# Performance work log

Measured on AMD Instinct MI355X. Metric: run time of the kernel, lower is better.

The kernel has to match this reference:

```python
import jax, jax.numpy as jnp
import numpy as np

C, H, OUT = 64, 128, 64          # in_channels, hidden_dim, out_channels
N, E = 20000, 640000             # nodes, edges
LN_EPS = 1e-5


def layer_norm(x, g, b):
    mu = jnp.mean(x, axis=-1, keepdims=True)
    var = jnp.var(x, axis=-1, keepdims=True)
    return (x - mu) * jax.lax.rsqrt(var + LN_EPS) * g + b


def setup_inputs() -> dict:
    key = jax.random.key(0)
    ks = jax.random.split(key, 12)
    F = 2 * C + 5  # edge MLP input dim = 133

    def w(k, shape, fan_in):
        return jax.random.normal(k, shape, jnp.float32) / np.float32(np.sqrt(fan_in))

    return {
        "x": jax.random.normal(ks[0], (N, C), jnp.float32),
        "pos": jax.random.normal(ks[1], (N, 2), jnp.float32),
        "vel": jax.random.normal(ks[2], (N, 2), jnp.float32),
        # phi_e: Linear(F,H) -> LN -> Softplus -> Linear(H,H) -> Softplus -> Linear(H,H)
        "We1": w(ks[3], (F, H), F), "be1": jnp.zeros((H,), jnp.float32),
        "ge1": jnp.ones((H,), jnp.float32), "bte1": jnp.zeros((H,), jnp.float32),
        "We2": w(ks[4], (H, H), H), "be2": jnp.zeros((H,), jnp.float32),
        "We3": w(ks[5], (H, H), H), "be3": jnp.zeros((H,), jnp.float32),
        # phi_v: Linear(F,H) -> LN -> Softplus -> Linear(H,1)
        "Wv1": w(ks[6], (F, H), F), "bv1": jnp.zeros((H,), jnp.float32),
        "gv1": jnp.ones((H,), jnp.float32), "btv1": jnp.zeros((H,), jnp.float32),
        "Wv2": w(ks[7], (H, 1), H), "bv2": jnp.zeros((1,), jnp.float32),
        # phi_h: Linear(C+H+1,H) -> LN -> Softplus -> Linear(H,OUT)
        "Wh1": w(ks[8], (C + H + 1, H), C + H + 1), "bh1": jnp.zeros((H,), jnp.float32),
        "gh1": jnp.ones((H,), jnp.float32), "bth1": jnp.zeros((H,), jnp.float32),
        "Wh2": w(ks[9], (H, OUT), H), "bh2": jnp.zeros((OUT,), jnp.float32),
        "edge_index": jax.random.randint(ks[10], (2, E), 0, N, dtype=jnp.int64)
        if jax.config.jax_enable_x64 else jax.random.randint(ks[10], (2, E), 0, N, dtype=jnp.int32),
    }


def reference(x, pos, vel,
              We1, be1, ge1, bte1, We2, be2, We3, be3,
              Wv1, bv1, gv1, btv1, Wv2, bv2,
              Wh1, bh1, gh1, bth1, Wh2, bh2,
              edge_index):
    src = edge_index[0]  # j (source / x_j)
    dst = edge_index[1]  # i (target / x_i, aggregation index)

    # per-edge geometric features (gather)
    rel_pos = pos[src] - pos[dst]                                   # [E,2]
    rel_vel = vel[src] - vel[dst]                                   # [E,2]
    dist_sq = jnp.sum(rel_pos ** 2, axis=-1, keepdims=True)         # [E,1]
    dot_vr = jnp.sum(rel_vel * rel_pos, axis=-1, keepdims=True)     # [E,1]
    r2_inv = jnp.minimum(1.0 / (dist_sq + 0.05), 20.0)
    r6_inv = jnp.minimum(r2_inv ** 3, 400.0)
    r12_inv = jnp.minimum(r6_inv ** 2, 160000.0)

    tmp = jnp.concatenate([x[dst], x[src], dist_sq, dot_vr,
                           r2_inv, r6_inv, r12_inv], axis=1)        # [E, 2C+5]

    # phi_e (edge MLP)
    h = jax.nn.softplus(layer_norm(tmp @ We1 + be1, ge1, bte1))
    h = jax.nn.softplus(h @ We2 + be2)
    m_h_e = h @ We3 + be3                                           # [E,H]

    # phi_v (scalar weight on rel_pos -> equivariant vector message)
    v = jax.nn.softplus(layer_norm(tmp @ Wv1 + bv1, gv1, btv1))
    v_w = v @ Wv2 + bv2                                             # [E,1]
    m_v_e = v_w * rel_pos                                           # [E,2]

    # scatter-mean aggregation to target nodes
    n_nodes = x.shape[0]
    ones = jnp.ones((src.shape[0], 1), x.dtype)
    cnt = jax.ops.segment_sum(ones, dst, num_segments=n_nodes)
    denom = jnp.maximum(cnt, 1.0)
    m_h = jax.ops.segment_sum(m_h_e, dst, num_segments=n_nodes) / denom   # [N,H]
    m_v = jax.ops.segment_sum(m_v_e, dst, num_segments=n_nodes) / denom   # [N,2]

    m_v_norm = jnp.sqrt(jnp.sum((m_v + 1e-8) ** 2, axis=-1, keepdims=True))  # [N,1]

    # phi_h (node update MLP); shortcut is Identity since C == OUT
    hin = jnp.concatenate([x, m_h, m_v_norm], axis=-1)              # [N, C+H+1]
    hu = jax.nn.softplus(layer_norm(hin @ Wh1 + bh1, gh1, bth1))
    h_update = hu @ Wh2 + bh2                                       # [N,OUT]
    return x + h_update
```

## Files before the change

kernel.cpp:

```cpp
#include <hip/hip_runtime.h>
#include <stdint.h>

#define NCH    64
#define HID    128
#define OUTC   64
#define NNODE  20000
#define NEDGE  640000
#define FDIM   133
#define PHIN   193
#define TE     32
#define TN     32
#define NST    36
#define LN_EPS 1e-5f
#define KP1    160
#define KP2    128
#define CAG    132

typedef __attribute__((ext_vector_type(8))) short bf16x8;
typedef __attribute__((ext_vector_type(4))) float f32x4;

__device__ __forceinline__ unsigned short f2bf(float f) {
    union { float f; unsigned int i; } v; v.f = f;
    unsigned int b = v.i;
    return (unsigned short)((b + 0x7FFFu + ((b >> 16) & 1u)) >> 16);
}
__device__ __forceinline__ float sp(float xv) {
    return fmaxf(xv, 0.f) + __logf(1.0f + __expf(-fabsf(xv)));
}
__device__ __forceinline__ void atomAddF(float* p, float v) {
    __hip_atomic_fetch_add(p, v, __ATOMIC_RELAXED, __HIP_MEMORY_SCOPE_AGENT);
}
__device__ __forceinline__ int fragOff(int ks, int mt, int lanepos) {
    return ((ks * 2 + mt) * 64 + lanepos) * 8;
}

#define WT_WE1 0
#define WT_WV1 (128 * KP1)
#define WT_WE2 (2 * 128 * KP1)
#define WT_WE3 (2 * 128 * KP1 + 128 * KP2)
#define WT_TOTAL (2 * 128 * KP1 + 2 * 128 * KP2)

__global__ __launch_bounds__(256)
void eg_prep(const float* __restrict__ We1, const float* __restrict__ Wv1,
             const float* __restrict__ We2, const float* __restrict__ We3,
             short* __restrict__ wt)
{
    int idx = blockIdx.x * 256 + threadIdx.x;
    if (idx >= WT_TOTAL) return;
    if (idx < WT_WV1) {
        int n = idx / KP1, k = idx % KP1;
        wt[idx] = (k < FDIM) ? (short)f2bf(We1[(size_t)k * HID + n]) : (short)0;
    } else if (idx < WT_WE2) {
        int r = idx - WT_WV1; int n = r / KP1, k = r % KP1;
        wt[idx] = (k < FDIM) ? (short)f2bf(Wv1[(size_t)k * HID + n]) : (short)0;
    } else if (idx < WT_WE3) {
        int r = idx - WT_WE2; int n = r / KP2, k = r % KP2;
        wt[idx] = (short)f2bf(We2[(size_t)k * HID + n]);
    } else {
        int r = idx - WT_WE3; int n = r / KP2, k = r % KP2;
        wt[idx] = (short)f2bf(We3[(size_t)k * HID + n]);
    }
}

__global__ __launch_bounds__(256)
void eg_hist(const int* __restrict__ ei, int* __restrict__ deg)
{
    int i = blockIdx.x * 256 + threadIdx.x;
    if (i < NEDGE)
        __hip_atomic_fetch_add(&deg[ei[NEDGE + i]], 1, __ATOMIC_RELAXED, __HIP_MEMORY_SCOPE_AGENT);
}

__global__ __launch_bounds__(1024)
void eg_scan(const int* __restrict__ deg, int* __restrict__ cur)
{
    __shared__ int part[1024];
    const int tid = threadIdx.x;
    const int chunk = (NNODE + 1023) / 1024;
    const int base = tid * chunk;
    const int lim = min(base + chunk, NNODE);
    int s = 0;
    for (int j = base; j < lim; ++j) s += deg[j];
    part[tid] = s;
    __syncthreads();
    for (int off = 1; off < 1024; off <<= 1) {
        int v = (tid >= off) ? part[tid - off] : 0;
        __syncthreads();
        part[tid] += v;
        __syncthreads();
    }
    int run = (tid > 0) ? part[tid - 1] : 0;
    for (int j = base; j < lim; ++j) { cur[j] = run; run += deg[j]; }
}

__global__ __launch_bounds__(256)
void eg_scatter(const int* __restrict__ ei, int* __restrict__ cur,
                int* __restrict__ perm)
{
    int i = blockIdx.x * 256 + threadIdx.x;
    if (i < NEDGE) {
        int d = ei[NEDGE + i];
        int p = __hip_atomic_fetch_add(&cur[d], 1, __ATOMIC_RELAXED, __HIP_MEMORY_SCOPE_AGENT);
        perm[p] = i;
    }
}

__global__ __launch_bounds__(256, 5)
void eg_edge(const float* __restrict__ x, const float* __restrict__ pos,
             const float* __restrict__ vel,
             const float* __restrict__ be1, const float* __restrict__ ge1,
             const float* __restrict__ bte1, const float* __restrict__ be2,
             const float* __restrict__ be3,
             const float* __restrict__ bv1, const float* __restrict__ gv1,
             const float* __restrict__ btv1,
             const float* __restrict__ Wv2, const float* __restrict__ bv2,
             const short* __restrict__ wt,
             const int* __restrict__ ei, const int* __restrict__ perm,
             float* __restrict__ mh, float* __restrict__ mv)
{
    __shared__ __align__(16) short frag_s[5 * 2 * 64 * 8];
    __shared__ __align__(16) float cagg_s[TE * CAG];
    __shared__ float psum_s[512];
    __shared__ float mu_s[64], rs_s[64];
    __shared__ int   dst_s[TE], src_s[TE];
    __shared__ float rel_s[TE * 2], vw_s[TE];

    const int tid  = threadIdx.x;
    const int lane = tid & 63;
    const int wid  = tid >> 6;
    const int lr   = lane & 15;
    const int quad = lane >> 4;
    const int n0w  = wid * 32;
    const int e_base = blockIdx.x * TE;

    const short* We1T = wt + WT_WE1;
    const short* Wv1T = wt + WT_WV1;
    const short* We2T = wt + WT_WE2;
    const short* We3T = wt + WT_WE3;

    float geo[5];
    if (tid < TE) {
        int gi = perm[e_base + tid];
        int eS = ei[gi];
        int eD = ei[NEDGE + gi];
        src_s[tid] = eS; dst_s[tid] = eD;
        float rx = pos[2 * eS]     - pos[2 * eD];
        float ry = pos[2 * eS + 1] - pos[2 * eD + 1];
        float vx = vel[2 * eS]     - vel[2 * eD];
        float vy = vel[2 * eS + 1] - vel[2 * eD + 1];
        float dsq = rx * rx + ry * ry;
        float dvr = vx * rx + vy * ry;
        float r2  = fminf(1.0f / (dsq + 0.05f), 20.0f);
        float r6  = fminf(r2 * r2 * r2, 400.0f);
        float r12 = fminf(r6 * r6, 160000.0f);
        geo[0] = dsq; geo[1] = dvr; geo[2] = r2; geo[3] = r6; geo[4] = r12;
        rel_s[2 * tid] = rx; rel_s[2 * tid + 1] = ry;
    }
    if (tid < 128) {
        int4 z = {0, 0, 0, 0};
        *(int4*)&frag_s[4 * 2 * 64 * 8 + tid * 8] = z;
    }
    __syncthreads();

    if (tid < TE) {
        int off = fragOff(4, tid >> 4, (tid & 15));
        #pragma unroll
        for (int j = 0; j < 5; ++j) frag_s[off + j] = (short)f2bf(geo[j]);
    }
    {
        const int e = tid & 31, slot = tid >> 5;
        const int d = dst_s[e], s = src_s[e];
        #pragma unroll
        for (int h = 0; h < 2; ++h) {
            int o = slot + h * 8;
            int node = h ? s : d;
            int c0 = (o & 7) * 8;
            const float4 a0 = *(const float4*)&x[(size_t)node * NCH + c0];
            const float4 a1 = *(const float4*)&x[(size_t)node * NCH + c0 + 4];
            bf16x8 v;
            v[0] = (short)f2bf(a0.x); v[1] = (short)f2bf(a0.y);
            v[2] = (short)f2bf(a0.z); v[3] = (short)f2bf(a0.w);
            v[4] = (short)f2bf(a1.x); v[5] = (short)f2bf(a1.y);
            v[6] = (short)f2bf(a1.z); v[7] = (short)f2bf(a1.w);
            int ks = o >> 2, kq = o & 3;
            *(bf16x8*)&frag_s[fragOff(ks, e >> 4, kq * 16 + (e & 15))] = v;
        }
    }
    __syncthreads();

    const int ncol0 = n0w + lr;
    const int ncol1 = n0w + 16 + lr;

    f32x4 zero4 = {0.f, 0.f, 0.f, 0.f};
    f32x4 accE[2][2], accV[2][2];
    #pragma unroll
    for (int mt = 0; mt < 2; ++mt)
        #pragma unroll
        for (int nt = 0; nt < 2; ++nt) { accE[mt][nt] = zero4; accV[mt][nt] = zero4; }
    for (int ks = 0; ks < 5; ++ks) {
        bf16x8 af0 = *(const bf16x8*)&frag_s[fragOff(ks, 0, lane)];
        bf16x8 af1 = *(const bf16x8*)&frag_s[fragOff(ks, 1, lane)];
        int krow = ks * 32 + quad * 8;
        #pragma unroll
        for (int nt = 0; nt < 2; ++nt) {
            int n = n0w + nt * 16 + lr;
            bf16x8 bwE = *(const bf16x8*)&We1T[n * KP1 + krow];
            bf16x8 bwV = *(const bf16x8*)&Wv1T[n * KP1 + krow];
            accE[0][nt] = __builtin_amdgcn_mfma_f32_16x16x32_bf16(af0, bwE, accE[0][nt], 0, 0, 0);
            accE[1][nt] = __builtin_amdgcn_mfma_f32_16x16x32_bf16(af1, bwE, accE[1][nt], 0, 0, 0);
            accV[0][nt] = __builtin_amdgcn_mfma_f32_16x16x32_bf16(af0, bwV, accV[0][nt], 0, 0, 0);
            accV[1][nt] = __builtin_amdgcn_mfma_f32_16x16x32_bf16(af1, bwV, accV[1][nt], 0, 0, 0);
        }
    }
    {
        float be0 = be1[ncol0], be_1 = be1[ncol1];
        float bv0 = bv1[ncol0], bv_1 = bv1[ncol1];
        #pragma unroll
        for (int mt = 0; mt < 2; ++mt)
            #pragma unroll
            for (int r = 0; r < 4; ++r) {
                accE[mt][0][r] += be0; accE[mt][1][r] += be_1;
                accV[mt][0][r] += bv0; accV[mt][1][r] += bv_1;
            }
    }

    #pragma unroll
    for (int mt = 0; mt < 2; ++mt)
        #pragma unroll
        for (int r = 0; r < 4; ++r) {
            float se = accE[mt][0][r] + accE[mt][1][r];
            float qe = accE[mt][0][r] * accE[mt][0][r] + accE[mt][1][r] * accE[mt][1][r];
            float sv = accV[mt][0][r] + accV[mt][1][r];
            float qv = accV[mt][0][r] * accV[mt][0][r] + accV[mt][1][r] * accV[mt][1][r];
            #pragma unroll
            for (int m = 1; m < 16; m <<= 1) {
                se += __shfl_xor(se, m, 16);
                qe += __shfl_xor(qe, m, 16);
                sv += __shfl_xor(sv, m, 16);
                qv += __shfl_xor(qv, m, 16);
            }
            if (lr == 0) {
                int row = mt * 16 + quad * 4 + r;
                psum_s[      row * 4 + wid] = se;
                psum_s[128 + row * 4 + wid] = qe;
                psum_s[256 + row * 4 + wid] = sv;
                psum_s[384 + row * 4 + wid] = qv;
            }
        }
    __syncthreads();
    if (tid < 64) {
        int p = tid >> 5, row = tid & 31;
        float s = 0.f, q = 0.f;
        #pragma unroll
        for (int w = 0; w < 4; ++w) {
            s += psum_s[p * 256 +       row * 4 + w];
            q += psum_s[p * 256 + 128 + row * 4 + w];
        }
        float mu = s * (1.0f / HID);
        float var = q * (1.0f / HID) - mu * mu;
        mu_s[p * 32 + row] = mu;
        rs_s[p * 32 + row] = rsqrtf(var + LN_EPS);
    }
    __syncthreads();

    {
        float gE0 = ge1[ncol0], gE1 = ge1[ncol1];
        float tE0 = bte1[ncol0], tE1 = bte1[ncol1];
        float gV0 = gv1[ncol0], gV1 = gv1[ncol1];
        float tV0 = btv1[ncol0], tV1 = btv1[ncol1];
        float w20 = Wv2[ncol0], w21 = Wv2[ncol1];
        int ks0 = ncol0 >> 5, kq0 = (ncol0 & 31) >> 3, j0 = ncol0 & 7;
        int ks1 = ncol1 >> 5, kq1 = (ncol1 & 31) >> 3, j1 = ncol1 & 7;
        int fo0 = (ks0 * 128 + kq0 * 16) * 8 + j0;
        int fo1 = (ks1 * 128 + kq1 * 16) * 8 + j1;
        #pragma unroll
        for (int mt = 0; mt < 2; ++mt)
            #pragma unroll
            for (int r = 0; r < 4; ++r) {
                int rlow = quad * 4 + r, row = mt * 16 + rlow;
                float mu = mu_s[row], rsv = rs_s[row];
                float muV = mu_s[32 + row], rsV = rs_s[32 + row];
                float h0 = sp((accE[mt][0][r] - mu) * rsv * gE0 + tE0);
                float h1 = sp((accE[mt][1][r] - mu) * rsv * gE1 + tE1);
                frag_s[fo0 + (mt * 64 + rlow) * 8] = (short)f2bf(h0);
                frag_s[fo1 + (mt * 64 + rlow) * 8] = (short)f2bf(h1);
                float v0 = sp((accV[mt][0][r] - muV) * rsV * gV0 + tV0);
                float v1 = sp((accV[mt][1][r] - muV) * rsV * gV1 + tV1);
                float vp = v0 * w20 + v1 * w21;
                #pragma unroll
                for (int m = 1; m < 16; m <<= 1) vp += __shfl_xor(vp, m, 16);
                if (lr == 0) psum_s[row * 4 + wid] = vp;
            }
    }
    __syncthreads();
    if (tid < TE) {
        float s = 0.f;
        #pragma unroll
        for (int w = 0; w < 4; ++w) s += psum_s[tid * 4 + w];
        vw_s[tid] = s + bv2[0];
    }

    {
        f32x4 acc2[2][2];
        #pragma unroll
        for (int mt = 0; mt < 2; ++mt)
            #pragma unroll
            for (int nt = 0; nt < 2; ++nt) acc2[mt][nt] = zero4;
        for (int ks = 0; ks < 4; ++ks) {
            bf16x8 af0 = *(const bf16x8*)&frag_s[fragOff(ks, 0, lane)];
            bf16x8 af1 = *(const bf16x8*)&frag_s[fragOff(ks, 1, lane)];
            int krow = ks * 32 + quad * 8;
            #pragma unroll
            for (int nt = 0; nt < 2; ++nt) {
                int n = n0w + nt * 16 + lr;
                bf16x8 bw = *(const bf16x8*)&We2T[n * KP2 + krow];
                acc2[0][nt] = __builtin_amdgcn_mfma_f32_16x16x32_bf16(af0, bw, acc2[0][nt], 0, 0, 0);
                acc2[1][nt] = __builtin_amdgcn_mfma_f32_16x16x32_bf16(af1, bw, acc2[1][nt], 0, 0, 0);
            }
        }
        __syncthreads();
        #pragma unroll
        for (int nt = 0; nt < 2; ++nt) {
            int kg = n0w + nt * 16 + lr;
            float b2 = be2[kg];
            int ks = kg >> 5, kq = (kg & 31) >> 3, j = kg & 7;
            #pragma unroll
            for (int mt = 0; mt < 2; ++mt)
                #pragma unroll
                for (int r = 0; r < 4; ++r) {
                    short v = (short)f2bf(sp(acc2[mt][nt][r] + b2));
                    frag_s[fragOff(ks, mt, kq * 16 + quad * 4 + r) + j] = v;
                }
        }
    }
    __syncthreads();

    {
        f32x4 acc3[2][2];
        #pragma unroll
        for (int mt = 0; mt < 2; ++mt)
            #pragma unroll
            for (int nt = 0; nt < 2; ++nt) acc3[mt][nt] = zero4;
        for (int ks = 0; ks < 4; ++ks) {
            bf16x8 af0 = *(const bf16x8*)&frag_s[fragOff(ks, 0, lane)];
            bf16x8 af1 = *(const bf16x8*)&frag_s[fragOff(ks, 1, lane)];
            int krow = ks * 32 + quad * 8;
            #pragma unroll
            for (int nt = 0; nt < 2; ++nt) {
                int n = n0w + nt * 16 + lr;
                bf16x8 bw = *(const bf16x8*)&We3T[n * KP2 + krow];
                acc3[0][nt] = __builtin_amdgcn_mfma_f32_16x16x32_bf16(af0, bw, acc3[0][nt], 0, 0, 0);
                acc3[1][nt] = __builtin_amdgcn_mfma_f32_16x16x32_bf16(af1, bw, acc3[1][nt], 0, 0, 0);
            }
        }
        #pragma unroll
        for (int nt = 0; nt < 2; ++nt) {
            int n = n0w + nt * 16 + lr;
            float b3 = be3[n];
            #pragma unroll
            for (int mt = 0; mt < 2; ++mt)
                #pragma unroll
                for (int r = 0; r < 4; ++r) {
                    int m = mt * 16 + quad * 4 + r;
                    cagg_s[m * CAG + n] = acc3[mt][nt][r] + b3;
                }
        }
    }
    __syncthreads();

    {
        const int c = tid & 127, h = tid >> 7;
        const int m0 = h * 16;
        float run = cagg_s[m0 * CAG + c];
        int curd = dst_s[m0];
        #pragma unroll
        for (int m = m0 + 1; m < m0 + 16; ++m) {
            int d = dst_s[m];
            float v = cagg_s[m * CAG + c];
            if (d == curd) run += v;
            else { atomAddF(&mh[(size_t)curd * HID + c], run); curd = d; run = v; }
        }
        atomAddF(&mh[(size_t)curd * HID + c], run);
    }
    if (tid < 2) {
        const int c = tid;
        float run = vw_s[0] * rel_s[c];
        int curd = dst_s[0];
        for (int m = 1; m < TE; ++m) {
            int d = dst_s[m];
            float v = vw_s[m] * rel_s[2 * m + c];
            if (d == curd) run += v;
            else { atomAddF(&mv[2 * curd + c], run); curd = d; run = v; }
        }
        atomAddF(&mv[2 * curd + c], run);
    }
}

__global__ __launch_bounds__(256)
void eg_node(const float* __restrict__ x,
             const float* __restrict__ Wh1, const float* __restrict__ bh1,
             const float* __restrict__ gh1, const float* __restrict__ bth1,
             const float* __restrict__ Wh2, const float* __restrict__ bh2,
             const float* __restrict__ mh, const float* __restrict__ mv,
             const int* __restrict__ deg, float* __restrict__ out)
{
    __shared__ float hin_s[PHIN * NST];
    __shared__ float H_s[HID * NST];
    __shared__ float den_s[TN], mu_s[TN], rs_s[TN];

    const int tid = threadIdx.x;
    const int n_base = blockIdx.x * TN;

    if (tid < TN) {
        int n = n_base + tid;
        float den = 1.f, norm = 0.f;
        if (n < NNODE) {
            den = fmaxf((float)deg[n], 1.0f);
            float ax = mv[2 * n] / den + 1e-8f;
            float ay = mv[2 * n + 1] / den + 1e-8f;
            norm = sqrtf(ax * ax + ay * ay);
        }
        den_s[tid] = den;
        hin_s[192 * NST + tid] = norm;
    }
    __syncthreads();
    {
        const int c = tid & 63, ng = tid >> 6;
        #pragma unroll
        for (int it = 0; it < 8; ++it) {
            int nl = it * 4 + ng;
            int n = n_base + nl;
            hin_s[c * NST + nl] = (n < NNODE) ? x[(size_t)n * NCH + c] : 0.f;
        }
        const int k = tid & 127, ng2 = tid >> 7;
        #pragma unroll
        for (int it = 0; it < 16; ++it) {
            int nl = it * 2 + ng2;
            int n = n_base + nl;
            hin_s[(NCH + k) * NST + nl] =
                (n < NNODE) ? mh[(size_t)n * HID + k] / den_s[nl] : 0.f;
        }
    }
    __syncthreads();

    const int n0 = (tid & 7) * 4;
    const int j0 = (tid >> 3) * 4;

    {
        float acc[4][4] = {};
        for (int k = 0; k < PHIN; ++k) {
            const float4 a = *(const float4*)&hin_s[k * NST + n0];
            const float4 wb = *(const float4*)(Wh1 + (size_t)k * HID + j0);
            const float w[4] = { wb.x, wb.y, wb.z, wb.w };
            const float aa[4] = { a.x, a.y, a.z, a.w };
            #pragma unroll
            for (int i = 0; i < 4; ++i)
                #pragma unroll
                for (int j = 0; j < 4; ++j) acc[i][j] += aa[i] * w[j];
        }
        #pragma unroll
        for (int j = 0; j < 4; ++j) {
            float b = bh1[j0 + j];
            #pragma unroll
            for (int i = 0; i < 4; ++i)
                H_s[(j0 + j) * NST + n0 + i] = acc[i][j] + b;
        }
    }
    __syncthreads();

    if (tid < TN) {
        float sum = 0.f, sq = 0.f;
        for (int k = 0; k < HID; ++k) {
            float v = H_s[k * NST + tid];
            sum += v; sq += v * v;
        }
        float mu = sum * (1.0f / HID);
        float var = sq * (1.0f / HID) - mu * mu;
        mu_s[tid] = mu;
        rs_s[tid] = rsqrtf(var + LN_EPS);
    }
    __syncthreads();
    {
        const int nl = tid & 31;
        const int jb = (tid >> 5) * 16;
        const float mu = mu_s[nl], rs = rs_s[nl];
        for (int jj = 0; jj < 16; ++jj) {
            int j = jb + jj;
            float v = H_s[j * NST + nl];
            v = (v - mu) * rs * gh1[j] + bth1[j];
            H_s[j * NST + nl] = sp(v);
        }
    }
    __syncthreads();

    {
        const int o0 = (tid >> 3) * 2;
        float acc[4][2] = {};
        for (int k = 0; k < HID; ++k) {
            const float4 a = *(const float4*)&H_s[k * NST + n0];
            const float2 wb = *(const float2*)(Wh2 + (size_t)k * OUTC + o0);
            const float aa[4] = { a.x, a.y, a.z, a.w };
            #pragma unroll
            for (int i = 0; i < 4; ++i) {
                acc[i][0] += aa[i] * wb.x;
                acc[i][1] += aa[i] * wb.y;
            }
        }
        #pragma unroll
        for (int jo = 0; jo < 2; ++jo) {
            float bo = bh2[o0 + jo];
            #pragma unroll
            for (int i = 0; i < 4; ++i) {
                int n = n_base + n0 + i;
                if (n < NNODE) {
                    out[(size_t)n * OUTC + o0 + jo] =
                        x[(size_t)n * NCH + o0 + jo] + acc[i][jo] + bo;
                }
            }
        }
    }
}

extern "C" void kernel_launch(void* const* d_in, const int* in_sizes, int n_in,
                              void* d_out, int out_size, void* d_ws, size_t ws_size,
                              hipStream_t stream)
{
    const float* x    = (const float*)d_in[0];
    const float* pos  = (const float*)d_in[1];
    const float* vel  = (const float*)d_in[2];
    const float* We1  = (const float*)d_in[3];
    const float* be1  = (const float*)d_in[4];
    const float* ge1  = (const float*)d_in[5];
    const float* bte1 = (const float*)d_in[6];
    const float* We2  = (const float*)d_in[7];
    const float* be2  = (const float*)d_in[8];
    const float* We3  = (const float*)d_in[9];
    const float* be3  = (const float*)d_in[10];
    const float* Wv1  = (const float*)d_in[11];
    const float* bv1  = (const float*)d_in[12];
    const float* gv1  = (const float*)d_in[13];
    const float* btv1 = (const float*)d_in[14];
    const float* Wv2  = (const float*)d_in[15];
    const float* bv2  = (const float*)d_in[16];
    const float* Wh1  = (const float*)d_in[17];
    const float* bh1  = (const float*)d_in[18];
    const float* gh1  = (const float*)d_in[19];
    const float* bth1 = (const float*)d_in[20];
    const float* Wh2  = (const float*)d_in[21];
    const float* bh2  = (const float*)d_in[22];
    const int*   ei   = (const int*)d_in[23];

    float* mh   = (float*)d_ws;
    float* mv   = mh + (size_t)NNODE * HID;
    int*   deg  = (int*)(mv + NNODE * 2);
    int*   cur  = deg + NNODE;
    int*   perm = cur + NNODE;
    short* wt   = (short*)(perm + NEDGE);

    size_t zbytes = ((size_t)NNODE * HID + NNODE * 2 + NNODE) * sizeof(float);
    hipMemsetAsync(d_ws, 0, zbytes, stream);

    eg_prep<<<dim3((WT_TOTAL + 255) / 256), dim3(256), 0, stream>>>(We1, Wv1, We2, We3, wt);
    eg_hist<<<dim3(NEDGE / 256), dim3(256), 0, stream>>>(ei, deg);
    eg_scan<<<dim3(1), dim3(1024), 0, stream>>>(deg, cur);
    eg_scatter<<<dim3(NEDGE / 256), dim3(256), 0, stream>>>(ei, cur, perm);

    eg_edge<<<dim3(NEDGE / TE), dim3(256), 0, stream>>>(
        x, pos, vel, be1, ge1, bte1, be2, be3,
        bv1, gv1, btv1, Wv2, bv2, wt, ei, perm, mh, mv);

    eg_node<<<dim3((NNODE + TN - 1) / TN), dim3(256), 0, stream>>>(
        x, Wh1, bh1, gh1, bth1, Wh2, bh2, mh, mv, deg, (float*)d_out);
}
```

Measured before the change: 598.5 us.

## Port node MLP to bf16 MFMA and shrink edge kernel LDS with bf16 staging

The node-update kernel moves from scalar fp32 FMA loops to bf16 MFMA tiles. It reuses the fragment layout of the edge kernel, with Wh1 and Wh2 pre-transposed into the weight workspace and LayerNorm done through wave shuffles. The edge kernel stores its per-edge message staging buffer as bf16 instead of fp32, uses packed bf16 conversion, and raises the occupancy hint from 5 to 7 blocks per CU. The costs are extra bf16 rounding in the aggregated messages and node MLP, and dropped bounds checks in the node kernel, which rely on N being a multiple of 32.

```diff
diff --git a/kernel.cpp b/kernel.cpp
--- a/kernel.cpp
+++ b/kernel.cpp
@@ -7,14 +7,13 @@
 #define NNODE  20000
 #define NEDGE  640000
 #define FDIM   133
-#define PHIN   193
 #define TE     32
 #define TN     32
-#define NST    36
 #define LN_EPS 1e-5f
 #define KP1    160
 #define KP2    128
-#define CAG    132
+#define KN1    224
+#define CAGS   130
 
 typedef __attribute__((ext_vector_type(8))) short bf16x8;
 typedef __attribute__((ext_vector_type(4))) float f32x4;
@@ -24,6 +23,22 @@
     unsigned int b = v.i;
     return (unsigned short)((b + 0x7FFFu + ((b >> 16) & 1u)) >> 16);
 }
+#if defined(__has_builtin)
+#if __has_builtin(__builtin_amdgcn_cvt_pk_bf16_f32)
+#define HAVE_PK_BF16 1
+#endif
+#endif
+__device__ __forceinline__ unsigned int f2bf_pk(float a, float b) {
+#ifdef HAVE_PK_BF16
+    auto r = __builtin_amdgcn_cvt_pk_bf16_f32(a, b);
+    return __builtin_bit_cast(unsigned int, r);
+#else
+    return (unsigned int)f2bf(a) | ((unsigned int)f2bf(b) << 16);
+#endif
+}
+__device__ __forceinline__ float bfu2f(unsigned short u) {
+    union { unsigned int i; float f; } v; v.i = ((unsigned int)u) << 16; return v.f;
+}
 __device__ __forceinline__ float sp(float xv) {
     return fmaxf(xv, 0.f) + __logf(1.0f + __expf(-fabsf(xv)));
 }
@@ -38,11 +53,14 @@
 #define WT_WV1 (128 * KP1)
 #define WT_WE2 (2 * 128 * KP1)
 #define WT_WE3 (2 * 128 * KP1 + 128 * KP2)
-#define WT_TOTAL (2 * 128 * KP1 + 2 * 128 * KP2)
+#define WT_WH1 (2 * 128 * KP1 + 2 * 128 * KP2)
+#define WT_WH2 (WT_WH1 + 128 * KN1)
+#define WT_TOTAL (WT_WH2 + 64 * KP2)
 
 __global__ __launch_bounds__(256)
 void eg_prep(const float* __restrict__ We1, const float* __restrict__ Wv1,
              const float* __restrict__ We2, const float* __restrict__ We3,
+             const float* __restrict__ Wh1, const float* __restrict__ Wh2,
              short* __restrict__ wt)
 {
     int idx = blockIdx.x * 256 + threadIdx.x;
@@ -56,9 +74,15 @@
     } else if (idx < WT_WE3) {
         int r = idx - WT_WE2; int n = r / KP2, k = r % KP2;
         wt[idx] = (short)f2bf(We2[(size_t)k * HID + n]);
-    } else {
+    } else if (idx < WT_WH1) {
         int r = idx - WT_WE3; int n = r / KP2, k = r % KP2;
         wt[idx] = (short)f2bf(We3[(size_t)k * HID + n]);
+    } else if (idx < WT_WH2) {
+        int r = idx - WT_WH1; int n = r / KN1, k = r % KN1;
+        wt[idx] = (k < 193) ? (short)f2bf(Wh1[(size_t)k * HID + n]) : (short)0;
+    } else {
+        int r = idx - WT_WH2; int n = r / KP2, k = r % KP2;
+        wt[idx] = (short)f2bf(Wh2[(size_t)k * OUTC + n]);
     }
 }
 
@@ -104,7 +128,7 @@
     }
 }
 
-__global__ __launch_bounds__(256, 5)
+__global__ __launch_bounds__(256, 7)
 void eg_edge(const float* __restrict__ x, const float* __restrict__ pos,
              const float* __restrict__ vel,
              const float* __restrict__ be1, const float* __restrict__ ge1,
@@ -118,7 +142,7 @@
              float* __restrict__ mh, float* __restrict__ mv)
 {
     __shared__ __align__(16) short frag_s[5 * 2 * 64 * 8];
-    __shared__ __align__(16) float cagg_s[TE * CAG];
+    __shared__ __align__(4) unsigned short cagg_s[TE * CAGS];
     __shared__ float psum_s[512];
     __shared__ float mu_s[64], rs_s[64];
     __shared__ int   dst_s[TE], src_s[TE];
@@ -176,13 +200,11 @@
             int c0 = (o & 7) * 8;
             const float4 a0 = *(const float4*)&x[(size_t)node * NCH + c0];
             const float4 a1 = *(const float4*)&x[(size_t)node * NCH + c0 + 4];
-            bf16x8 v;
-            v[0] = (short)f2bf(a0.x); v[1] = (short)f2bf(a0.y);
-            v[2] = (short)f2bf(a0.z); v[3] = (short)f2bf(a0.w);
-            v[4] = (short)f2bf(a1.x); v[5] = (short)f2bf(a1.y);
-            v[6] = (short)f2bf(a1.z); v[7] = (short)f2bf(a1.w);
+            uint4 pk;
+            pk.x = f2bf_pk(a0.x, a0.y); pk.y = f2bf_pk(a0.z, a0.w);
+            pk.z = f2bf_pk(a1.x, a1.y); pk.w = f2bf_pk(a1.z, a1.w);
             int ks = o >> 2, kq = o & 3;
-            *(bf16x8*)&frag_s[fragOff(ks, e >> 4, kq * 16 + (e & 15))] = v;
+            *(uint4*)&frag_s[fragOff(ks, e >> 4, kq * 16 + (e & 15))] = pk;
         }
     }
     __syncthreads();
@@ -281,8 +303,9 @@
                 float muV = mu_s[32 + row], rsV = rs_s[32 + row];
                 float h0 = sp((accE[mt][0][r] - mu) * rsv * gE0 + tE0);
                 float h1 = sp((accE[mt][1][r] - mu) * rsv * gE1 + tE1);
-                frag_s[fo0 + (mt * 64 + rlow) * 8] = (short)f2bf(h0);
-                frag_s[fo1 + (mt * 64 + rlow) * 8] = (short)f2bf(h1);
+                unsigned int ph = f2bf_pk(h0, h1);
+                frag_s[fo0 + (mt * 64 + rlow) * 8] = (short)(ph & 0xFFFFu);
+                frag_s[fo1 + (mt * 64 + rlow) * 8] = (short)(ph >> 16);
                 float v0 = sp((accV[mt][0][r] - muV) * rsV * gV0 + tV0);
                 float v1 = sp((accV[mt][1][r] - muV) * rsV * gV1 + tV1);
                 float vp = v0 * w20 + v1 * w21;
@@ -324,12 +347,14 @@
             float b2 = be2[kg];
             int ks = kg >> 5, kq = (kg & 31) >> 3, j = kg & 7;
             #pragma unroll
-            for (int mt = 0; mt < 2; ++mt)
-                #pragma unroll
-                for (int r = 0; r < 4; ++r) {
-                    short v = (short)f2bf(sp(acc2[mt][nt][r] + b2));
-                    frag_s[fragOff(ks, mt, kq * 16 + quad * 4 + r) + j] = v;
-                }
+            for (int mt = 0; mt < 2; ++mt) {
+                unsigned int u0 = f2bf_pk(sp(acc2[mt][nt][0] + b2), sp(acc2[mt][nt][1] + b2));
+                unsigned int u1 = f2bf_pk(sp(acc2[mt][nt][2] + b2), sp(acc2[mt][nt][3] + b2));
+                frag_s[fragOff(ks, mt, kq * 16 + quad * 4 + 0) + j] = (short)(u0 & 0xFFFFu);
+                frag_s[fragOff(ks, mt, kq * 16 + quad * 4 + 1) + j] = (short)(u0 >> 16);
+                frag_s[fragOff(ks, mt, kq * 16 + quad * 4 + 2) + j] = (short)(u1 & 0xFFFFu);
+                frag_s[fragOff(ks, mt, kq * 16 + quad * 4 + 3) + j] = (short)(u1 >> 16);
+            }
         }
     }
     __syncthreads();
@@ -357,12 +382,15 @@
             int n = n0w + nt * 16 + lr;
             float b3 = be3[n];
             #pragma unroll
-            for (int mt = 0; mt < 2; ++mt)
-                #pragma unroll
-                for (int r = 0; r < 4; ++r) {
-                    int m = mt * 16 + quad * 4 + r;
-                    cagg_s[m * CAG + n] = acc3[mt][nt][r] + b3;
-                }
+            for (int mt = 0; mt < 2; ++mt) {
+                int mb = mt * 16 + quad * 4;
+                unsigned int u0 = f2bf_pk(acc3[mt][nt][0] + b3, acc3[mt][nt][1] + b3);
+                unsigned int u1 = f2bf_pk(acc3[mt][nt][2] + b3, acc3[mt][nt][3] + b3);
+                cagg_s[(mb + 0) * CAGS + n] = (unsigned short)(u0 & 0xFFFFu);
+                cagg_s[(mb + 1) * CAGS + n] = (unsigned short)(u0 >> 16);
+                cagg_s[(mb + 2) * CAGS + n] = (unsigned short)(u1 & 0xFFFFu);
+                cagg_s[(mb + 3) * CAGS + n] = (unsigned short)(u1 >> 16);
+            }
         }
     }
     __syncthreads();
@@ -370,12 +398,12 @@
     {
         const int c = tid & 127, h = tid >> 7;
         const int m0 = h * 16;
-        float run = cagg_s[m0 * CAG + c];
+        float run = bfu2f(cagg_s[m0 * CAGS + c]);
         int curd = dst_s[m0];
         #pragma unroll
         for (int m = m0 + 1; m < m0 + 16; ++m) {
             int d = dst_s[m];
-            float v = cagg_s[m * CAG + c];
+            float v = bfu2f(cagg_s[m * CAGS + c]);
             if (d == curd) run += v;
             else { atomAddF(&mh[(size_t)curd * HID + c], run); curd = d; run = v; }
         }
@@ -395,128 +423,180 @@
     }
 }
 
-__global__ __launch_bounds__(256)
+__global__ __launch_bounds__(256, 7)
 void eg_node(const float* __restrict__ x,
-             const float* __restrict__ Wh1, const float* __restrict__ bh1,
-             const float* __restrict__ gh1, const float* __restrict__ bth1,
-             const float* __restrict__ Wh2, const float* __restrict__ bh2,
+             const float* __restrict__ bh1, const float* __restrict__ gh1,
+             const float* __restrict__ bth1, const float* __restrict__ bh2,
              const float* __restrict__ mh, const float* __restrict__ mv,
-             const int* __restrict__ deg, float* __restrict__ out)
+             const int* __restrict__ deg, const short* __restrict__ wt,
+             float* __restrict__ out)
 {
-    __shared__ float hin_s[PHIN * NST];
-    __shared__ float H_s[HID * NST];
-    __shared__ float den_s[TN], mu_s[TN], rs_s[TN];
-
-    const int tid = threadIdx.x;
+    __shared__ __align__(16) short frag_s[7 * 2 * 64 * 8];
+    __shared__ float psum_s[256];
+    __shared__ float mu_s[32], rs_s[32];
+    __shared__ float rden_s[TN], norm_s[TN];
+
+    const int tid  = threadIdx.x;
+    const int lane = tid & 63;
+    const int wid  = tid >> 6;
+    const int lr   = lane & 15;
+    const int quad = lane >> 4;
+    const int n0w  = wid * 32;
     const int n_base = blockIdx.x * TN;
+
+    const short* Wh1T = wt + WT_WH1;
+    const short* Wh2T = wt + WT_WH2;
 
     if (tid < TN) {
         int n = n_base + tid;
-        float den = 1.f, norm = 0.f;
-        if (n < NNODE) {
-            den = fmaxf((float)deg[n], 1.0f);
-            float ax = mv[2 * n] / den + 1e-8f;
-            float ay = mv[2 * n + 1] / den + 1e-8f;
-            norm = sqrtf(ax * ax + ay * ay);
-        }
-        den_s[tid] = den;
-        hin_s[192 * NST + tid] = norm;
-    }
-    __syncthreads();
-    {
-        const int c = tid & 63, ng = tid >> 6;
-        #pragma unroll
-        for (int it = 0; it < 8; ++it) {
-            int nl = it * 4 + ng;
-            int n = n_base + nl;
-            hin_s[c * NST + nl] = (n < NNODE) ? x[(size_t)n * NCH + c] : 0.f;
-        }
-        const int k = tid & 127, ng2 = tid >> 7;
-        #pragma unroll
-        for (int it = 0; it < 16; ++it) {
-            int nl = it * 2 + ng2;
-            int n = n_base + nl;
-            hin_s[(NCH + k) * NST + nl] =
-                (n < NNODE) ? mh[(size_t)n * HID + k] / den_s[nl] : 0.f;
-        }
-    }
-    __syncthreads();
-
-    const int n0 = (tid & 7) * 4;
-    const int j0 = (tid >> 3) * 4;
-
-    {
-        float acc[4][4] = {};
-        for (int k = 0; k < PHIN; ++k) {
-            const float4 a = *(const float4*)&hin_s[k * NST + n0];
-            const float4 wb = *(const float4*)(Wh1 + (size_t)k * HID + j0);
-            const float w[4] = { wb.x, wb.y, wb.z, wb.w };
-            const float aa[4] = { a.x, a.y, a.z, a.w };
-            #pragma unroll
-            for (int i = 0; i < 4; ++i)
-                #pragma unroll
-                for (int j = 0; j < 4; ++j) acc[i][j] += aa[i] * w[j];
-        }
-        #pragma unroll
-        for (int j = 0; j < 4; ++j) {
-            float b = bh1[j0 + j];
-            #pragma unroll
-            for (int i = 0; i < 4; ++i)
-                H_s[(j0 + j) * NST + n0 + i] = acc[i][j] + b;
-        }
-    }
-    __syncthreads();
-
+        float den = fmaxf((float)deg[n], 1.0f);
+        float rd = 1.0f / den;
+        float ax = mv[2 * n] * rd + 1e-8f;
+        float ay = mv[2 * n + 1] * rd + 1e-8f;
+        rden_s[tid] = rd;
+        norm_s[tid] = sqrtf(ax * ax + ay * ay);
+    }
+    if (tid < 128) {
+        int4 z = {0, 0, 0, 0};
+        *(int4*)&frag_s[6 * 2 * 64 * 8 + tid * 8] = z;
+    }
+    __syncthreads();
+
+    {
+        const int e = tid & 31, slot = tid >> 5;
+        const int n = n_base + e;
+        {
+            int c0 = slot * 8;
+            const float4 a0 = *(const float4*)&x[(size_t)n * NCH + c0];
+            const float4 a1 = *(const float4*)&x[(size_t)n * NCH + c0 + 4];
+            uint4 pk;
+            pk.x = f2bf_pk(a0.x, a0.y); pk.y = f2bf_pk(a0.z, a0.w);
+            pk.z = f2bf_pk(a1.x, a1.y); pk.w = f2bf_pk(a1.z, a1.w);
+            int ks = slot >> 2, kq = slot & 3;
+            *(uint4*)&frag_s[fragOff(ks, e >> 4, kq * 16 + (e & 15))] = pk;
+        }
+        float rd = rden_s[e];
+        #pragma unroll
+        for (int h = 0; h < 2; ++h) {
+            int o = 8 + slot + h * 8;
+            int k0 = (o - 8) * 8;
+            const float4 a0 = *(const float4*)&mh[(size_t)n * HID + k0];
+            const float4 a1 = *(const float4*)&mh[(size_t)n * HID + k0 + 4];
+            uint4 pk;
+            pk.x = f2bf_pk(a0.x * rd, a0.y * rd); pk.y = f2bf_pk(a0.z * rd, a0.w * rd);
+            pk.z = f2bf_pk(a1.x * rd, a1.y * rd); pk.w = f2bf_pk(a1.z * rd, a1.w * rd);
+            int ks = o >> 2, kq = o & 3;
+            *(uint4*)&frag_s[fragOff(ks, e >> 4, kq * 16 + (e & 15))] = pk;
+        }
+    }
     if (tid < TN) {
-        float sum = 0.f, sq = 0.f;
-        for (int k = 0; k < HID; ++k) {
-            float v = H_s[k * NST + tid];
-            sum += v; sq += v * v;
-        }
-        float mu = sum * (1.0f / HID);
-        float var = sq * (1.0f / HID) - mu * mu;
+        frag_s[fragOff(6, tid >> 4, (tid & 15))] = (short)f2bf(norm_s[tid]);
+    }
+    __syncthreads();
+
+    const int ncol0 = n0w + lr;
+    const int ncol1 = n0w + 16 + lr;
+
+    f32x4 zero4 = {0.f, 0.f, 0.f, 0.f};
+    f32x4 acc1[2][2];
+    #pragma unroll
+    for (int mt = 0; mt < 2; ++mt)
+        #pragma unroll
+        for (int nt = 0; nt < 2; ++nt) acc1[mt][nt] = zero4;
+    for (int ks = 0; ks < 7; ++ks) {
+        bf16x8 af0 = *(const bf16x8*)&frag_s[fragOff(ks, 0, lane)];
+        bf16x8 af1 = *(const bf16x8*)&frag_s[fragOff(ks, 1, lane)];
+        int krow = ks * 32 + quad * 8;
+        #pragma unroll
+        for (int nt = 0; nt < 2; ++nt) {
+            int n = n0w + nt * 16 + lr;
+            bf16x8 bw = *(const bf16x8*)&Wh1T[n * KN1 + krow];
+            acc1[0][nt] = __builtin_amdgcn_mfma_f32_16x16x32_bf16(af0, bw, acc1[0][nt], 0, 0, 0);
+            acc1[1][nt] = __builtin_amdgcn_mfma_f32_16x16x32_bf16(af1, bw, acc1[1][nt], 0, 0, 0);
+        }
+    }
+    {
+        float b0 = bh1[ncol0], b1 = bh1[ncol1];
+        #pragma unroll
+        for (int mt = 0; mt < 2; ++mt)
+            #pragma unroll
+            for (int r = 0; r < 4; ++r) { acc1[mt][0][r] += b0; acc1[mt][1][r] += b1; }
+    }
+
+    #pragma unroll
+    for (int mt = 0; mt < 2; ++mt)
+        #pragma unroll
+        for (int r = 0; r < 4; ++r) {
+            float s = acc1[mt][0][r] + acc1[mt][1][r];
+            float q = acc1[mt][0][r] * acc1[mt][0][r] + acc1[mt][1][r] * acc1[mt][1][r];
+            #pragma unroll
+            for (int m = 1; m < 16; m <<= 1) {
+                s += __shfl_xor(s, m, 16);
+                q += __shfl_xor(q, m, 16);
+            }
+            if (lr == 0) {
+                int row = mt * 16 + quad * 4 + r;
+                psum_s[row * 4 + wid]       = s;
+                psum_s[128 + row * 4 + wid] = q;
+            }
+        }
+    __syncthreads();
+    if (tid < 32) {
+        float s = 0.f, q = 0.f;
+        #pragma unroll
+        for (int w = 0; w < 4; ++w) {
+            s += psum_s[tid * 4 + w];
+            q += psum_s[128 + tid * 4 + w];
+        }
+        float mu = s * (1.0f / HID);
+        float var = q * (1.0f / HID) - mu * mu;
         mu_s[tid] = mu;
         rs_s[tid] = rsqrtf(var + LN_EPS);
     }
     __syncthreads();
-    {
-        const int nl = tid & 31;
-        const int jb = (tid >> 5) * 16;
-        const float mu = mu_s[nl], rs = rs_s[nl];
-        for (int jj = 0; jj < 16; ++jj) {
-            int j = jb + jj;
-            float v = H_s[j * NST + nl];
-            v = (v - mu) * rs * gh1[j] + bth1[j];
-            H_s[j * NST + nl] = sp(v);
-        }
-    }
-    __syncthreads();
-
-    {
-        const int o0 = (tid >> 3) * 2;
-        float acc[4][2] = {};
-        for (int k = 0; k < HID; ++k) {
-            const float4 a = *(const float4*)&H_s[k * NST + n0];
-            const float2 wb = *(const float2*)(Wh2 + (size_t)k * OUTC + o0);
-            const float aa[4] = { a.x, a.y, a.z, a.w };
-            #pragma unroll
-            for (int i = 0; i < 4; ++i) {
-                acc[i][0] += aa[i] * wb.x;
-                acc[i][1] += aa[i] * wb.y;
-            }
-        }
-        #pragma unroll
-        for (int jo = 0; jo < 2; ++jo) {
-            float bo = bh2[o0 + jo];
-            #pragma unroll
-            for (int i = 0; i < 4; ++i) {
-                int n = n_base + n0 + i;
-                if (n < NNODE) {
-                    out[(size_t)n * OUTC + o0 + jo] =
-                        x[(size_t)n * NCH + o0 + jo] + acc[i][jo] + bo;
-                }
-            }
-        }
+
+    {
+        float g0 = gh1[ncol0], g1 = gh1[ncol1];
+        float t0 = bth1[ncol0], t1 = bth1[ncol1];
+        int ks0 = ncol0 >> 5, kq0 = (ncol0 & 31) >> 3, j0 = ncol0 & 7;
+        int ks1 = ncol1 >> 5, kq1 = (ncol1 & 31) >> 3, j1 = ncol1 & 7;
+        int fo0 = (ks0 * 128 + kq0 * 16) * 8 + j0;
+        int fo1 = (ks1 * 128 + kq1 * 16) * 8 + j1;
+        #pragma unroll
+        for (int mt = 0; mt < 2; ++mt)
+            #pragma unroll
+            for (int r = 0; r < 4; ++r) {
+                int rlow = quad * 4 + r, row = mt * 16 + rlow;
+                float mu = mu_s[row], rsv = rs_s[row];
+                float h0 = sp((acc1[mt][0][r] - mu) * rsv * g0 + t0);
+                float h1 = sp((acc1[mt][1][r] - mu) * rsv * g1 + t1);
+                unsigned int ph = f2bf_pk(h0, h1);
+                frag_s[fo0 + (mt * 64 + rlow) * 8] = (short)(ph & 0xFFFFu);
+                frag_s[fo1 + (mt * 64 + rlow) * 8] = (short)(ph >> 16);
+            }
+    }
+    __syncthreads();
+
+    {
+        const int col = wid * 16 + lr;
+        f32x4 acc2[2] = { zero4, zero4 };
+        for (int ks = 0; ks < 4; ++ks) {
+            bf16x8 af0 = *(const bf16x8*)&frag_s[fragOff(ks, 0, lane)];
+            bf16x8 af1 = *(const bf16x8*)&frag_s[fragOff(ks, 1, lane)];
+            int krow = ks * 32 + quad * 8;
+            bf16x8 bw = *(const bf16x8*)&Wh2T[col * KP2 + krow];
+            acc2[0] = __builtin_amdgcn_mfma_f32_16x16x32_bf16(af0, bw, acc2[0], 0, 0, 0);
+            acc2[1] = __builtin_amdgcn_mfma_f32_16x16x32_bf16(af1, bw, acc2[1], 0, 0, 0);
+        }
+        float bo = bh2[col];
+        #pragma unroll
+        for (int mt = 0; mt < 2; ++mt)
+            #pragma unroll
+            for (int r = 0; r < 4; ++r) {
+                int m = mt * 16 + quad * 4 + r;
+                size_t idx = (size_t)(n_base + m) * OUTC + col;
+                out[idx] = x[(size_t)(n_base + m) * NCH + col] + acc2[mt][r] + bo;
+            }
     }
 }
 
@@ -559,7 +639,8 @@
     size_t zbytes = ((size_t)NNODE * HID + NNODE * 2 + NNODE) * sizeof(float);
     hipMemsetAsync(d_ws, 0, zbytes, stream);
 
-    eg_prep<<<dim3((WT_TOTAL + 255) / 256), dim3(256), 0, stream>>>(We1, Wv1, We2, We3, wt);
+    eg_prep<<<dim3((WT_TOTAL + 255) / 256), dim3(256), 0, stream>>>(
+        We1, Wv1, We2, We3, Wh1, Wh2, wt);
     eg_hist<<<dim3(NEDGE / 256), dim3(256), 0, stream>>>(ei, deg);
     eg_scan<<<dim3(1), dim3(1024), 0, stream>>>(deg, cur);
     eg_scatter<<<dim3(NEDGE / 256), dim3(256), 0, stream>>>(ei, cur, perm);
@@ -568,6 +649,6 @@
         x, pos, vel, be1, ge1, bte1, be2, be3,
         bv1, gv1, btv1, Wv2, bv2, wt, ei, perm, mh, mv);
 
-    eg_node<<<dim3((NNODE + TN - 1) / TN), dim3(256), 0, stream>>>(
-        x, Wh1, bh1, gh1, bth1, Wh2, bh2, mh, mv, deg, (float*)d_out);
-}
+    eg_node<<<dim3(NNODE / TN), dim3(256), 0, stream>>>(
+        x, bh1, gh1, bth1, bh2, mh, mv, deg, wt, (float*)d_out);
+}
```

Measured after the change: 542.5 us. -9.4%, faster.
